# Kernel optimization log

Hardware: AMD Instinct MI355X
Metric: run time of the kernel (lower is better)

Reference implementation:

```python
import jax, jax.numpy as jnp
import numpy as np

B, S, D = 2, 2048, 2048
N_HEADS = 16
HEAD_DIM = D // N_HEADS  # 128


def apply_rotary(xq, xk, cos, sin):
    # xq, xk: [B, S, H, HD]; cos, sin: [S, HD//2]
    def rot(t):
        tr = t.reshape(t.shape[:-1] + (HEAD_DIM // 2, 2))
        r, i = tr[..., 0], tr[..., 1]
        c = cos[None, :, None, :]  # [1, S, 1, HD//2]
        s = sin[None, :, None, :]
        out_r = r * c - i * s
        out_i = r * s + i * c
        return jnp.stack([out_r, out_i], axis=-1).reshape(t.shape)
    return rot(xq), rot(xk)


def setup_inputs() -> dict:
    key = jax.random.key(0)
    k1, k2, k3 = jax.random.split(key, 3)
    x = jax.random.normal(k1, (B, S, D), dtype=jnp.float32)
    wqkv = jax.random.normal(k2, (3 * D, D), dtype=jnp.float32) * (D ** -0.5)
    wo = jax.random.normal(k3, (D, D), dtype=jnp.float32) * (D ** -0.5)
    # rotary tables, standard llama theta=10000
    inv_freq = 1.0 / (10000.0 ** (jnp.arange(0, HEAD_DIM, 2, dtype=jnp.float32) / HEAD_DIM))
    t = jnp.arange(S, dtype=jnp.float32)
    freqs = jnp.outer(t, inv_freq)  # [S, HD//2]
    freqs_cos = jnp.cos(freqs)
    freqs_sin = jnp.sin(freqs)
    # causal additive mask [1, 1, S, S]
    causal = jnp.tril(jnp.ones((S, S), dtype=bool))
    mask = jnp.where(causal, 0.0, -jnp.inf).astype(jnp.float32)[None, None]
    return {"x": x, "freqs_cos": freqs_cos, "freqs_sin": freqs_sin,
            "mask": mask, "wqkv": wqkv, "wo": wo, "input_pos": 0}


def reference(x, freqs_cos, freqs_sin, mask, wqkv, wo, input_pos):
    # fused QKV projection (Linear: x @ W^T)
    qkv = jnp.einsum('bsd,ed->bse', x, wqkv)  # [B, S, 3D]
    xq, xk, xv = jnp.split(qkv, 3, axis=-1)
    xq = xq.reshape(B, S, N_HEADS, HEAD_DIM)
    xk = xk.reshape(B, S, N_HEADS, HEAD_DIM)
    xv = xv.reshape(B, S, N_HEADS, HEAD_DIM)
    xq, xk = apply_rotary(xq, xk, freqs_cos, freqs_sin)
    # SDPA (kv_cache is None; input_pos unused)
    scale = HEAD_DIM ** -0.5
    scores = jnp.einsum('bqhd,bkhd->bhqk', xq, xk) * scale + mask
    attn = jax.nn.softmax(scores, axis=-1)
    out = jnp.einsum('bhqk,bkhd->bqhd', attn, xv).reshape(B, S, D)
    return jnp.einsum('bsd,ed->bse', out, wo)
```

## Files before the change

kernel.cpp:

```cpp
#include <hip/hip_runtime.h>

#define B_ 2
#define S_ 2048
#define D_ 2048
#define H_ 16
#define DH_ 128
#define E3_ (3*D_)

typedef __attribute__((ext_vector_type(4))) float f32x4;
typedef __attribute__((ext_vector_type(8))) short bf16x8;

__device__ __forceinline__ unsigned short f2bf(float f) {
  unsigned u = __float_as_uint(f);
  u += 0x7fff + ((u >> 16) & 1);
  return (unsigned short)(u >> 16);
}
__device__ __forceinline__ float bf2f(unsigned short h) {
  return __uint_as_float(((unsigned)h) << 16);
}
__device__ __forceinline__ unsigned cvt_pk_bf16(float lo, float hi) {
  unsigned r;
  asm("v_cvt_pk_bf16_f32 %0, %1, %2" : "=v"(r) : "v"(lo), "v"(hi));
  return r;
}

__global__ void cast_f32_bf16(const float* __restrict__ in, unsigned short* __restrict__ out, int n4) {
  int i = blockIdx.x * 256 + threadIdx.x;
  if (i >= n4) return;
  float4 v = reinterpret_cast<const float4*>(in)[i];
  ushort4 o;
  o.x = f2bf(v.x); o.y = f2bf(v.y); o.z = f2bf(v.z); o.w = f2bf(v.w);
  reinterpret_cast<ushort4*>(out)[i] = o;
}

template<typename OutT>
__global__ __launch_bounds__(256) void gemm_bt(const unsigned short* __restrict__ A,
                                               const unsigned short* __restrict__ Bm,
                                               OutT* __restrict__ C,
                                               unsigned short* __restrict__ Vt,
                                               int Mdim, int Ndim, int Kdim) {
  __shared__ __align__(16) unsigned short As[128*64];
  __shared__ __align__(16) unsigned short Bs[128*64];
  const int t = threadIdx.x;
  const int lane = t & 63;
  const int w = t >> 6;
  const int wm = w >> 1, wn = w & 1;
  const int l16 = lane & 15, lg = lane >> 4;
  const int bm = blockIdx.y, bn = blockIdx.x;

  f32x4 acc[4][4] = {};
  const int e0 = t * 8;

  for (int k0 = 0; k0 < Kdim; k0 += 64) {
#pragma unroll
    for (int it = 0; it < 4; ++it) {
      int e = e0 + it * 2048;
      int row = e >> 6;
      int g = (e >> 3) & 7;
      int gs = g ^ (row & 7);
      const unsigned short* ga = A  + (size_t)(bm*128 + row) * Kdim + k0 + gs*8;
      const unsigned short* gb = Bm + (size_t)(bn*128 + row) * Kdim + k0 + gs*8;
      __builtin_amdgcn_global_load_lds((const __attribute__((address_space(1))) unsigned int*)ga,
                                       (__attribute__((address_space(3))) unsigned int*)(&As[e]), 16, 0, 0);
      __builtin_amdgcn_global_load_lds((const __attribute__((address_space(1))) unsigned int*)gb,
                                       (__attribute__((address_space(3))) unsigned int*)(&Bs[e]), 16, 0, 0);
    }
    __syncthreads();
#pragma unroll
    for (int kk = 0; kk < 2; ++kk) {
      bf16x8 a[4], b[4];
#pragma unroll
      for (int mi = 0; mi < 4; ++mi) {
        int row = wm*64 + mi*16 + l16;
        int gw = kk*4 + lg;
        a[mi] = *reinterpret_cast<const bf16x8*>(&As[row*64 + ((gw ^ (row & 7))<<3)]);
      }
#pragma unroll
      for (int ni = 0; ni < 4; ++ni) {
        int row = wn*64 + ni*16 + l16;
        int gw = kk*4 + lg;
        b[ni] = *reinterpret_cast<const bf16x8*>(&Bs[row*64 + ((gw ^ (row & 7))<<3)]);
      }
#pragma unroll
      for (int mi = 0; mi < 4; ++mi)
#pragma unroll
        for (int ni = 0; ni < 4; ++ni)
          acc[mi][ni] = __builtin_amdgcn_mfma_f32_16x16x32_bf16(a[mi], b[ni], acc[mi][ni], 0, 0, 0);
    }
    __syncthreads();
  }
  if constexpr (sizeof(OutT) == 2) {
    if (Vt != nullptr && bn >= 32) {
#pragma unroll
      for (int mi = 0; mi < 4; ++mi) {
#pragma unroll
        for (int ni = 0; ni < 4; ++ni) {
          int colv = bn*128 + wn*64 + ni*16 + l16 - 2*D_;
          int h = colv >> 7, d = colv & 127;
          int row0 = bm*128 + wm*64 + mi*16 + lg*4;
          int b = row0 >> 11, s = row0 & 2047;
          ushort4 v4;
          v4.x = f2bf(acc[mi][ni][0]);
          v4.y = f2bf(acc[mi][ni][1]);
          v4.z = f2bf(acc[mi][ni][2]);
          v4.w = f2bf(acc[mi][ni][3]);
          *reinterpret_cast<ushort4*>(&Vt[(((size_t)(b*H_ + h))*DH_ + d)*S_ + s]) = v4;
        }
      }
      return;
    }
  }
#pragma unroll
  for (int mi = 0; mi < 4; ++mi) {
#pragma unroll
    for (int ni = 0; ni < 4; ++ni) {
      int col = bn*128 + wn*64 + ni*16 + l16;
      int row0 = bm*128 + wm*64 + mi*16 + lg*4;
#pragma unroll
      for (int r = 0; r < 4; ++r) {
        float v = acc[mi][ni][r];
        size_t idx = (size_t)(row0 + r) * Ndim + col;
        if constexpr (sizeof(OutT) == 2) C[idx] = f2bf(v);
        else C[idx] = v;
      }
    }
  }
}

__global__ void rope_qk(const unsigned short* __restrict__ qkv,
                        const float* __restrict__ cosT, const float* __restrict__ sinT,
                        unsigned short* __restrict__ Q, unsigned short* __restrict__ K) {
  const float SCL = 0.08838834764831845f * 1.4426950408889634f;
  int d = threadIdx.x;
  int h = blockIdx.x;
  int s = blockIdx.y;
  int b = blockIdx.z;
  size_t rowb = ((size_t)(b*S_ + s)) * E3_;
  int j = d >> 1;
  float c  = cosT[s*64 + j];
  float sn = sinT[s*64 + j];
  int de = d & ~1, odd = d & 1;
  float x0 = bf2f(qkv[rowb + h*DH_ + de]);
  float x1 = bf2f(qkv[rowb + h*DH_ + de + 1]);
  float oq = odd ? (x0*sn + x1*c) : (x0*c - x1*sn);
  size_t qo = (((size_t)(b*H_ + h)) * S_ + s) * DH_ + d;
  Q[qo] = f2bf(oq * SCL);
  float y0 = bf2f(qkv[rowb + D_ + h*DH_ + de]);
  float y1 = bf2f(qkv[rowb + D_ + h*DH_ + de + 1]);
  float ok = odd ? (y0*sn + y1*c) : (y0*c - y1*sn);
  K[qo] = f2bf(ok);
}

#define NQT 32
__global__ __launch_bounds__(512) void attn(const unsigned short* __restrict__ Q,
                                            const unsigned short* __restrict__ K,
                                            const unsigned short* __restrict__ Vt,
                                            unsigned short* __restrict__ O) {
  __shared__ __align__(16) unsigned short Ks[64*128];
  __shared__ __align__(16) unsigned short Vs[128*64];
  __shared__ __align__(16) unsigned short Plds[8][16*64];
  const int x = blockIdx.x;
  const int bh = blockIdx.y;
  const int b = bh >> 4, h = bh & 15;
  const int t = threadIdx.x;
  const int lane = t & 63;
  const int w = t >> 6;
  const int wg = w >> 2;
  const int wi = w & 3;
  const int l16 = lane & 15, lg = lane >> 4;
  const int qt = wg ? (NQT - 1 - x) : x;
  const int q0 = qt * 64 + wi * 16;
  const unsigned short* Qh = Q  + (size_t)bh * S_ * DH_;
  const unsigned short* Kh = K  + (size_t)bh * S_ * DH_;
  const unsigned short* Vh = Vt + (size_t)bh * DH_ * S_;

  bf16x8 aq[4];
#pragma unroll
  for (int kk = 0; kk < 4; ++kk)
    aq[kk] = *reinterpret_cast<const bf16x8*>(Qh + (size_t)(q0 + l16)*DH_ + kk*32 + lg*8);

  f32x4 o[8] = {};
  float mrun = -1e30f, lrun = 0.f;
  const int ntiles = NQT - x;

  for (int tile = 0; tile < ntiles; ++tile) {
    const int kv0 = tile * 64;
#pragma unroll
    for (int it = 0; it < 2; ++it) {
      int e = t*8 + it*4096;
      int row = e >> 7;
      int gslot = (e >> 3) & 15;
      int gsrc = gslot ^ (row & 7);
      const unsigned short* ga = Kh + (size_t)(kv0 + row) * DH_ + gsrc*8;
      __builtin_amdgcn_global_load_lds((const __attribute__((address_space(1))) unsigned int*)ga,
                                       (__attribute__((address_space(3))) unsigned int*)(&Ks[e]), 16, 0, 0);
    }
#pragma unroll
    for (int it = 0; it < 2; ++it) {
      int e = t*8 + it*4096;
      int d = e >> 6;
      int gslot = (e >> 3) & 7;
      int gsrc = gslot ^ (d & 7);
      const unsigned short* gv = Vh + (size_t)d * S_ + kv0 + gsrc*8;
      __builtin_amdgcn_global_load_lds((const __attribute__((address_space(1))) unsigned int*)gv,
                                       (__attribute__((address_space(3))) unsigned int*)(&Vs[e]), 16, 0, 0);
    }
    __syncthreads();

    if (tile <= qt) {
      f32x4 sc[4] = {};
#pragma unroll
      for (int kk = 0; kk < 4; ++kk) {
#pragma unroll
        for (int n = 0; n < 4; ++n) {
          int row = n*16 + l16;
          int g = kk*4 + lg;
          bf16x8 bk = *reinterpret_cast<const bf16x8*>(&Ks[row*128 + ((g ^ (row & 7))<<3)]);
          sc[n] = __builtin_amdgcn_mfma_f32_16x16x32_bf16(bk, aq[kk], sc[n], 0, 0, 0);
        }
      }
      if (tile == qt) {
        int qrow = q0 + l16;
#pragma unroll
        for (int n = 0; n < 4; ++n)
#pragma unroll
          for (int r = 0; r < 4; ++r) {
            int kidx = kv0 + n*16 + lg*4 + r;
            sc[n][r] = (kidx > qrow) ? -1e30f : sc[n][r];
          }
      }
      float mt = sc[0][0];
#pragma unroll
      for (int n = 0; n < 4; ++n)
#pragma unroll
        for (int r = 0; r < 4; ++r) mt = fmaxf(mt, sc[n][r]);
      mt = fmaxf(mt, __shfl_xor(mt, 16));
      mt = fmaxf(mt, __shfl_xor(mt, 32));
      if (__any(mt > mrun + 8.f)) {
        float mnew = fmaxf(mrun, mt);
        float alpha = __builtin_amdgcn_exp2f(mrun - mnew);
        mrun = mnew;
        lrun *= alpha;
        float ar[4];
#pragma unroll
        for (int r = 0; r < 4; ++r) ar[r] = __shfl(alpha, lg*4 + r);
#pragma unroll
        for (int n2 = 0; n2 < 8; ++n2)
#pragma unroll
          for (int r = 0; r < 4; ++r) o[n2][r] *= ar[r];
      }
      float rs = 0.f;
      unsigned pk[4][2];
#pragma unroll
      for (int n = 0; n < 4; ++n) {
        float p0 = __builtin_amdgcn_exp2f(sc[n][0] - mrun);
        float p1 = __builtin_amdgcn_exp2f(sc[n][1] - mrun);
        float p2 = __builtin_amdgcn_exp2f(sc[n][2] - mrun);
        float p3 = __builtin_amdgcn_exp2f(sc[n][3] - mrun);
        rs += (p0 + p1) + (p2 + p3);
        pk[n][0] = cvt_pk_bf16(p0, p1);
        pk[n][1] = cvt_pk_bf16(p2, p3);
      }
      rs += __shfl_xor(rs, 16);
      rs += __shfl_xor(rs, 32);
      lrun += rs;
      unsigned short* Pw = &Plds[w][0];
      char* Pb = (char*)Pw + l16*128;
#pragma unroll
      for (int n = 0; n < 4; ++n) {
        int sslot = (n*4 + lg) ^ (l16 & 14);
        *reinterpret_cast<uint2*>(Pb + sslot*8) = make_uint2(pk[n][0], pk[n][1]);
      }
      bf16x8 pa[2];
#pragma unroll
      for (int kk2 = 0; kk2 < 2; ++kk2) {
        int tp = (kk2*4 + lg) ^ ((l16 >> 1) & 7);
        pa[kk2] = *reinterpret_cast<const bf16x8*>(Pb + tp*16);
      }
#pragma unroll
      for (int kk2 = 0; kk2 < 2; ++kk2) {
#pragma unroll
        for (int n2 = 0; n2 < 8; ++n2) {
          int d = n2*16 + l16;
          int g = kk2*4 + lg;
          bf16x8 bv = *reinterpret_cast<const bf16x8*>(&Vs[d*64 + ((g ^ (d & 7))<<3)]);
          o[n2] = __builtin_amdgcn_mfma_f32_16x16x32_bf16(pa[kk2], bv, o[n2], 0, 0, 0);
        }
      }
    }
    __syncthreads();
  }
  float linv = 1.f / lrun;
  float lr[4];
#pragma unroll
  for (int r = 0; r < 4; ++r) lr[r] = __shfl(linv, lg*4 + r);
  size_t ob = ((size_t)b * S_) * D_;
#pragma unroll
  for (int n2 = 0; n2 < 8; ++n2) {
#pragma unroll
    for (int r = 0; r < 4; ++r) {
      int rowq = q0 + lg*4 + r;
      int d = n2*16 + l16;
      O[ob + (size_t)rowq * D_ + h*DH_ + d] = f2bf(o[n2][r] * lr[r]);
    }
  }
}

extern "C" void kernel_launch(void* const* d_in, const int* in_sizes, int n_in,
                              void* d_out, int out_size, void* d_ws, size_t ws_size,
                              hipStream_t stream) {
  const float* x    = (const float*)d_in[0];
  const float* fcos = (const float*)d_in[1];
  const float* fsin = (const float*)d_in[2];
  const float* wqkv = (const float*)d_in[4];
  const float* wo   = (const float*)d_in[5];
  float* out = (float*)d_out;
  char* ws = (char*)d_ws;

  unsigned short* xb    = (unsigned short*)(ws);
  unsigned short* wqkvb = (unsigned short*)(ws + 16777216);
  unsigned short* wob   = (unsigned short*)(ws + 41943040);
  unsigned short* qkv   = (unsigned short*)(ws + 50331648);
  unsigned short* Qb    = (unsigned short*)(ws + 100663296);
  unsigned short* Kb    = (unsigned short*)(ws + 117440512);
  unsigned short* Vtb   = (unsigned short*)(ws + 134217728);
  unsigned short* attn_out = xb;

  cast_f32_bf16<<<dim3(2097152/256), 256, 0, stream>>>(x, xb, 2097152);
  cast_f32_bf16<<<dim3(3145728/256), 256, 0, stream>>>(wqkv, wqkvb, 3145728);
  cast_f32_bf16<<<dim3(1048576/256), 256, 0, stream>>>(wo, wob, 1048576);

  gemm_bt<unsigned short><<<dim3(6144/128, 4096/128), 256, 0, stream>>>(xb, wqkvb, qkv, Vtb, 4096, 6144, 2048);
  rope_qk<<<dim3(16, 2048, 2), 128, 0, stream>>>(qkv, fcos, fsin, Qb, Kb);
  attn<<<dim3(16, 32), 512, 0, stream>>>(Qb, Kb, Vtb, attn_out);
  gemm_bt<float><<<dim3(2048/128, 4096/128), 256, 0, stream>>>(attn_out, wob, out, (unsigned short*)nullptr, 4096, 2048, 2048);
}
```

Baseline: 271.2 us.

## Double-buffer KV tiles in attention, vectorize RoPE, remap blocks, add MFMA priority

The attention kernel now double-buffers its K and V tiles in LDS. It issues the async global-to-LDS loads for the next tile before computing the current one and drops one barrier per iteration. It also remaps block ids so consecutive workgroups are spread across heads, and raises wave priority around the MFMA loops. Separately, rope_qk is rewritten so each thread handles 8 contiguous elements with vector loads and stores, one block per token. These changes cost twice the LDS for K/V, which may lower occupancy.

```diff
diff --git a/kernel.cpp b/kernel.cpp
--- a/kernel.cpp
+++ b/kernel.cpp
@@ -127,28 +127,47 @@
   }
 }
 
-__global__ void rope_qk(const unsigned short* __restrict__ qkv,
-                        const float* __restrict__ cosT, const float* __restrict__ sinT,
-                        unsigned short* __restrict__ Q, unsigned short* __restrict__ K) {
-  const float SCL = 0.08838834764831845f * 1.4426950408889634f;
-  int d = threadIdx.x;
-  int h = blockIdx.x;
-  int s = blockIdx.y;
-  int b = blockIdx.z;
-  size_t rowb = ((size_t)(b*S_ + s)) * E3_;
-  int j = d >> 1;
-  float c  = cosT[s*64 + j];
-  float sn = sinT[s*64 + j];
-  int de = d & ~1, odd = d & 1;
-  float x0 = bf2f(qkv[rowb + h*DH_ + de]);
-  float x1 = bf2f(qkv[rowb + h*DH_ + de + 1]);
-  float oq = odd ? (x0*sn + x1*c) : (x0*c - x1*sn);
-  size_t qo = (((size_t)(b*H_ + h)) * S_ + s) * DH_ + d;
-  Q[qo] = f2bf(oq * SCL);
-  float y0 = bf2f(qkv[rowb + D_ + h*DH_ + de]);
-  float y1 = bf2f(qkv[rowb + D_ + h*DH_ + de + 1]);
-  float ok = odd ? (y0*sn + y1*c) : (y0*c - y1*sn);
-  K[qo] = f2bf(ok);
+__global__ __launch_bounds__(256) void rope_qk(const unsigned short* __restrict__ qkv,
+                                               const float* __restrict__ cosT,
+                                               const float* __restrict__ sinT,
+                                               unsigned short* __restrict__ Q,
+                                               unsigned short* __restrict__ K) {
+  const float SCLQ = 0.08838834764831845f * 1.4426950408889634f;
+  const int idx = blockIdx.x;
+  const int b = idx >> 11, s = idx & 2047;
+  const int t = threadIdx.x;
+  const int e = t * 8;
+  const int h = e >> 7, d0 = e & 127;
+  const int j0 = d0 >> 1;
+  const size_t rowb = (size_t)(b*S_ + s) * E3_;
+  float4 c4 = *reinterpret_cast<const float4*>(&cosT[s*64 + j0]);
+  float4 s4 = *reinterpret_cast<const float4*>(&sinT[s*64 + j0]);
+  float cc[4] = {c4.x, c4.y, c4.z, c4.w};
+  float ss[4] = {s4.x, s4.y, s4.z, s4.w};
+  const size_t qo = (((size_t)(b*H_ + h)) * S_ + s) * DH_ + d0;
+
+  ushort4 qv[2], kv[2], qd[2], kd[2];
+  qv[0] = *reinterpret_cast<const ushort4*>(&qkv[rowb + e]);
+  qv[1] = *reinterpret_cast<const ushort4*>(&qkv[rowb + e + 4]);
+  kv[0] = *reinterpret_cast<const ushort4*>(&qkv[rowb + D_ + e]);
+  kv[1] = *reinterpret_cast<const ushort4*>(&qkv[rowb + D_ + e + 4]);
+#pragma unroll
+  for (int p = 0; p < 4; ++p) {
+    unsigned short* qi = (unsigned short*)&qv[p >> 1] + (p & 1) * 2;
+    unsigned short* ki = (unsigned short*)&kv[p >> 1] + (p & 1) * 2;
+    unsigned short* qo2 = (unsigned short*)&qd[p >> 1] + (p & 1) * 2;
+    unsigned short* ko2 = (unsigned short*)&kd[p >> 1] + (p & 1) * 2;
+    float x0 = bf2f(qi[0]), x1 = bf2f(qi[1]);
+    qo2[0] = f2bf((x0*cc[p] - x1*ss[p]) * SCLQ);
+    qo2[1] = f2bf((x0*ss[p] + x1*cc[p]) * SCLQ);
+    float y0 = bf2f(ki[0]), y1 = bf2f(ki[1]);
+    ko2[0] = f2bf(y0*cc[p] - y1*ss[p]);
+    ko2[1] = f2bf(y0*ss[p] + y1*cc[p]);
+  }
+  *reinterpret_cast<ushort4*>(&Q[qo])     = qd[0];
+  *reinterpret_cast<ushort4*>(&Q[qo + 4]) = qd[1];
+  *reinterpret_cast<ushort4*>(&K[qo])     = kd[0];
+  *reinterpret_cast<ushort4*>(&K[qo + 4]) = kd[1];
 }
 
 #define NQT 32
@@ -156,19 +175,21 @@
                                             const unsigned short* __restrict__ K,
                                             const unsigned short* __restrict__ Vt,
                                             unsigned short* __restrict__ O) {
-  __shared__ __align__(16) unsigned short Ks[64*128];
-  __shared__ __align__(16) unsigned short Vs[128*64];
+  __shared__ __align__(16) unsigned short Ks[2][64*128];
+  __shared__ __align__(16) unsigned short Vs[2][128*64];
   __shared__ __align__(16) unsigned short Plds[8][16*64];
-  const int x = blockIdx.x;
-  const int bh = blockIdx.y;
+  const int orig = blockIdx.y * gridDim.x + blockIdx.x;
+  const int wgid = (orig & 7) * 64 + (orig >> 3);
+  const int x = wgid & 15;
+  const int bh = wgid >> 4;
   const int b = bh >> 4, h = bh & 15;
   const int t = threadIdx.x;
   const int lane = t & 63;
   const int w = t >> 6;
-  const int wg = w >> 2;
+  const int wg8 = w >> 2;
   const int wi = w & 3;
   const int l16 = lane & 15, lg = lane >> 4;
-  const int qt = wg ? (NQT - 1 - x) : x;
+  const int qt = wg8 ? (NQT - 1 - x) : x;
   const int q0 = qt * 64 + wi * 16;
   const unsigned short* Qh = Q  + (size_t)bh * S_ * DH_;
   const unsigned short* Kh = K  + (size_t)bh * S_ * DH_;
@@ -183,42 +204,55 @@
   float mrun = -1e30f, lrun = 0.f;
   const int ntiles = NQT - x;
 
+#define STAGE_KV(TILE)                                                                              \
+  {                                                                                                 \
+    const int kv0s = (TILE) * 64;                                                                   \
+    unsigned short* Kd = &Ks[(TILE) & 1][0];                                                        \
+    unsigned short* Vd = &Vs[(TILE) & 1][0];                                                        \
+    _Pragma("unroll")                                                                               \
+    for (int it = 0; it < 2; ++it) {                                                                \
+      int e = t*8 + it*4096;                                                                        \
+      int row = e >> 7;                                                                             \
+      int gslot = (e >> 3) & 15;                                                                    \
+      int gsrc = gslot ^ (row & 7);                                                                 \
+      const unsigned short* ga = Kh + (size_t)(kv0s + row) * DH_ + gsrc*8;                          \
+      __builtin_amdgcn_global_load_lds((const __attribute__((address_space(1))) unsigned int*)ga,   \
+                                       (__attribute__((address_space(3))) unsigned int*)(&Kd[e]), 16, 0, 0); \
+    }                                                                                               \
+    _Pragma("unroll")                                                                               \
+    for (int it = 0; it < 2; ++it) {                                                                \
+      int e = t*8 + it*4096;                                                                        \
+      int dd = e >> 6;                                                                              \
+      int gslot = (e >> 3) & 7;                                                                     \
+      int gsrc = gslot ^ (dd & 7);                                                                  \
+      const unsigned short* gv = Vh + (size_t)dd * S_ + kv0s + gsrc*8;                              \
+      __builtin_amdgcn_global_load_lds((const __attribute__((address_space(1))) unsigned int*)gv,   \
+                                       (__attribute__((address_space(3))) unsigned int*)(&Vd[e]), 16, 0, 0); \
+    }                                                                                               \
+  }
+
+  STAGE_KV(0);
+
   for (int tile = 0; tile < ntiles; ++tile) {
+    __syncthreads();
+    if (tile + 1 < ntiles) STAGE_KV(tile + 1);
     const int kv0 = tile * 64;
-#pragma unroll
-    for (int it = 0; it < 2; ++it) {
-      int e = t*8 + it*4096;
-      int row = e >> 7;
-      int gslot = (e >> 3) & 15;
-      int gsrc = gslot ^ (row & 7);
-      const unsigned short* ga = Kh + (size_t)(kv0 + row) * DH_ + gsrc*8;
-      __builtin_amdgcn_global_load_lds((const __attribute__((address_space(1))) unsigned int*)ga,
-                                       (__attribute__((address_space(3))) unsigned int*)(&Ks[e]), 16, 0, 0);
-    }
-#pragma unroll
-    for (int it = 0; it < 2; ++it) {
-      int e = t*8 + it*4096;
-      int d = e >> 6;
-      int gslot = (e >> 3) & 7;
-      int gsrc = gslot ^ (d & 7);
-      const unsigned short* gv = Vh + (size_t)d * S_ + kv0 + gsrc*8;
-      __builtin_amdgcn_global_load_lds((const __attribute__((address_space(1))) unsigned int*)gv,
-                                       (__attribute__((address_space(3))) unsigned int*)(&Vs[e]), 16, 0, 0);
-    }
-    __syncthreads();
+    const int buf = tile & 1;
 
     if (tile <= qt) {
       f32x4 sc[4] = {};
+      __builtin_amdgcn_s_setprio(1);
 #pragma unroll
       for (int kk = 0; kk < 4; ++kk) {
 #pragma unroll
         for (int n = 0; n < 4; ++n) {
           int row = n*16 + l16;
           int g = kk*4 + lg;
-          bf16x8 bk = *reinterpret_cast<const bf16x8*>(&Ks[row*128 + ((g ^ (row & 7))<<3)]);
+          bf16x8 bk = *reinterpret_cast<const bf16x8*>(&Ks[buf][row*128 + ((g ^ (row & 7))<<3)]);
           sc[n] = __builtin_amdgcn_mfma_f32_16x16x32_bf16(bk, aq[kk], sc[n], 0, 0, 0);
         }
       }
+      __builtin_amdgcn_s_setprio(0);
       if (tile == qt) {
         int qrow = q0 + l16;
 #pragma unroll
@@ -277,18 +311,19 @@
         int tp = (kk2*4 + lg) ^ ((l16 >> 1) & 7);
         pa[kk2] = *reinterpret_cast<const bf16x8*>(Pb + tp*16);
       }
+      __builtin_amdgcn_s_setprio(1);
 #pragma unroll
       for (int kk2 = 0; kk2 < 2; ++kk2) {
 #pragma unroll
         for (int n2 = 0; n2 < 8; ++n2) {
           int d = n2*16 + l16;
           int g = kk2*4 + lg;
-          bf16x8 bv = *reinterpret_cast<const bf16x8*>(&Vs[d*64 + ((g ^ (d & 7))<<3)]);
+          bf16x8 bv = *reinterpret_cast<const bf16x8*>(&Vs[buf][d*64 + ((g ^ (d & 7))<<3)]);
           o[n2] = __builtin_amdgcn_mfma_f32_16x16x32_bf16(pa[kk2], bv, o[n2], 0, 0, 0);
         }
       }
-    }
-    __syncthreads();
+      __builtin_amdgcn_s_setprio(0);
+    }
   }
   float linv = 1.f / lrun;
   float lr[4];
@@ -330,8 +365,8 @@
   cast_f32_bf16<<<dim3(3145728/256), 256, 0, stream>>>(wqkv, wqkvb, 3145728);
   cast_f32_bf16<<<dim3(1048576/256), 256, 0, stream>>>(wo, wob, 1048576);
 
-  gemm_bt<unsigned short><<<dim3(6144/128, 4096/128), 256, 0, stream>>>(xb, wqkvb, qkv, Vtb, 4096, 6144, 2048);
-  rope_qk<<<dim3(16, 2048, 2), 128, 0, stream>>>(qkv, fcos, fsin, Qb, Kb);
+  gemm_bt<unsigned short><<<dim3(48, 32), 256, 0, stream>>>(xb, wqkvb, qkv, Vtb, 4096, 6144, 2048);
+  rope_qk<<<dim3(4096), 256, 0, stream>>>(qkv, fcos, fsin, Qb, Kb);
   attn<<<dim3(16, 32), 512, 0, stream>>>(Qb, Kb, Vtb, attn_out);
-  gemm_bt<float><<<dim3(2048/128, 4096/128), 256, 0, stream>>>(attn_out, wob, out, (unsigned short*)nullptr, 4096, 2048, 2048);
-}
+  gemm_bt<float><<<dim3(16, 32), 256, 0, stream>>>(attn_out, wob, out, (unsigned short*)nullptr, 4096, 2048, 2048);
+}
```

Measured after the change: 260.6 us. 1.04x faster.
